# Optimization experiments

Hardware: AMD Instinct MI355X
Metric: run time of the kernel (lower is better)

## Reference

```python
import jax, jax.numpy as jnp
import numpy as np
from jax import lax

B, OBS, E, H = 65536, 20, 64, 64


def setup_inputs() -> dict:
    key = jax.random.key(0)
    ks = jax.random.split(key, 13)
    s = 0.1
    inp = {
        "obs_traj": jax.random.normal(ks[0], (B, OBS, 2), jnp.float32),
        "W_emb": jax.random.normal(ks[1], (E, 2), jnp.float32) * s,
        "b_emb": jax.random.normal(ks[2], (E,), jnp.float32) * s,
        "Wih_e": jax.random.normal(ks[3], (4 * H, E), jnp.float32) * s,
        "Whh_e": jax.random.normal(ks[4], (4 * H, H), jnp.float32) * s,
        "bih_e": jax.random.normal(ks[5], (4 * H,), jnp.float32) * s,
        "bhh_e": jax.random.normal(ks[6], (4 * H,), jnp.float32) * s,
        "Wih_d": jax.random.normal(ks[7], (4 * H, E), jnp.float32) * s,
        "Whh_d": jax.random.normal(ks[8], (4 * H, H), jnp.float32) * s,
        "bih_d": jax.random.normal(ks[9], (4 * H,), jnp.float32) * s,
        "bhh_d": jax.random.normal(ks[10], (4 * H,), jnp.float32) * s,
        "W_fc": jax.random.normal(ks[11], (2, H), jnp.float32) * s,
        "b_fc": jax.random.normal(ks[12], (2,), jnp.float32) * s,
        "pred_len": 12,
    }
    return inp


def _lstm_step(x, h, c, Wih, Whh, b):
    # PyTorch LSTM gate order: i, f, g, o
    g = x @ Wih.T + h @ Whh.T + b  # [B, 4H]
    i, f, gg, o = jnp.split(g, 4, axis=-1)
    c2 = jax.nn.sigmoid(f) * c + jax.nn.sigmoid(i) * jnp.tanh(gg)
    h2 = jax.nn.sigmoid(o) * jnp.tanh(c2)
    return h2, c2


def reference(obs_traj, W_emb, b_emb, Wih_e, Whh_e, bih_e, bhh_e,
              Wih_d, Whh_d, bih_d, bhh_d, W_fc, b_fc, pred_len):
    bsz = obs_traj.shape[0]
    dt = obs_traj.dtype
    # Encoder: embed all observed steps at once, then scan the LSTM over time.
    emb = jax.nn.relu(obs_traj @ W_emb.T + b_emb)  # [B, OBS, E]
    b_e = bih_e + bhh_e
    h0 = jnp.zeros((bsz, H), dt)
    c0 = jnp.zeros((bsz, H), dt)

    def enc_step(carry, x_t):
        h, c = carry
        h, c = _lstm_step(x_t, h, c, Wih_e, Whh_e, b_e)
        return (h, c), None

    (h, c), _ = lax.scan(enc_step, (h0, c0), jnp.swapaxes(emb, 0, 1))

    b_d = bih_d + bhh_d
    dec_in = jax.nn.relu(obs_traj[:, -1, :] @ W_emb.T + b_emb)  # [B, E]

    def dec_step(carry, _):
        h, c, x = carry
        h, c = _lstm_step(x, h, c, Wih_d, Whh_d, b_d)
        pred = h @ W_fc.T + b_fc  # [B, 2]
        nxt = jax.nn.relu(pred @ W_emb.T + b_emb)
        return (h, c, nxt), pred

    _, preds = lax.scan(dec_step, (h, c, dec_in), None, length=pred_len)
    return jnp.swapaxes(preds, 0, 1)  # [B, pred_len, 2]
```

## Files before the change

kernel.cpp:

```cpp
#include <hip/hip_runtime.h>

typedef __bf16 bf16x8 __attribute__((ext_vector_type(8)));
typedef __bf16 bf16x4 __attribute__((ext_vector_type(4)));
typedef float  f32x4  __attribute__((ext_vector_type(4)));
typedef float  f32x2  __attribute__((ext_vector_type(2)));

constexpr int BATCH = 65536;
constexpr int OBS   = 20;
constexpr int PRED  = 12;
constexpr int BT    = 64;
constexpr int AST   = 136;

constexpr float SIO = -1.4426950408889634f;
constexpr float SG  =  2.8853900817779268f;

__device__ __forceinline__ float exp2_(float x) { return __builtin_amdgcn_exp2f(x); }
__device__ __forceinline__ float rcp_(float x)  { return __builtin_amdgcn_rcpf(x); }

struct SmallW {
    float  biasf_e[256];
    float  biasf_d[256];
    float4 embc[64];
    float  wfc[128];
    float  bfc[2];
};

__global__ __launch_bounds__(256, 3)
void vanilla_lstm(const float* __restrict__ obs,
                  const float* __restrict__ W_emb, const float* __restrict__ b_emb,
                  const float* __restrict__ Wih_e, const float* __restrict__ Whh_e,
                  const float* __restrict__ bih_e, const float* __restrict__ bhh_e,
                  const float* __restrict__ Wih_d, const float* __restrict__ Whh_d,
                  const float* __restrict__ bih_d, const float* __restrict__ bhh_d,
                  const float* __restrict__ W_fc,  const float* __restrict__ b_fc,
                  float* __restrict__ out)
{
    __shared__ __align__(16) __bf16 As[BT * AST];
    __shared__ bf16x8 wkt3[1024];
    __shared__ __align__(16) float  pred_s[BT * 2];
    __shared__ SmallW sw;

    const int tid  = threadIdx.x;
    const int wv   = tid >> 6;
    const int lane = tid & 63;
    const int m    = lane & 15;
    const int q    = lane >> 4;
    const int wblk = wv * 16;
    const size_t gRow0 = (size_t)blockIdx.x * BT;

    {
        const int wv_ = tid >> 6, c_ = (tid >> 4) & 3, qr = tid & 15;
        const int g = c_ * 64 + wv_ * 16 + qr;
        const float sc = (c_ == 2) ? SG : SIO;
        sw.biasf_e[tid] = sc * (bih_e[g] + bhh_e[g]);
        sw.biasf_d[tid] = sc * (bih_d[g] + bhh_d[g]);
    }
    if (tid < 64)  sw.embc[tid] = make_float4(W_emb[2 * tid], W_emb[2 * tid + 1], b_emb[tid], 0.f);
    if (tid < 128) sw.wfc[tid]  = W_fc[tid];
    if (tid < 2)   sw.bfc[tid]  = b_fc[tid];

    {
        uint4 z; z.x = z.y = z.z = z.w = 0u;
        uint4* p = (uint4*)As;
        constexpr int NV = BT * AST * 2 / 16;
        #pragma unroll
        for (int i = 0; i < NV / 256; ++i) p[tid + i * 256] = z;
        if (tid < (NV % 256)) p[tid + (NV / 256) * 256] = z;
    }

    bf16x8 bfr[4][3];
    auto load_bfr = [&](const float* Wih, const float* Whh) {
        #pragma unroll
        for (int c = 0; c < 4; ++c) {
            const float sc = (c == 2) ? SG : SIO;
            const int n = c * 64 + wblk + m;
            #pragma unroll
            for (int kt = 0; kt < 3; ++kt) {
                const float* s = (kt < 2) ? (Wih + n * 64 + kt * 32 + q * 8)
                                          : (Whh + n * 64 + q * 8);
                float4 a = *(const float4*)s;
                float4 b = *(const float4*)(s + 4);
                bf16x8 v;
                v[0] = (__bf16)(sc * a.x); v[1] = (__bf16)(sc * a.y);
                v[2] = (__bf16)(sc * a.z); v[3] = (__bf16)(sc * a.w);
                v[4] = (__bf16)(sc * b.x); v[5] = (__bf16)(sc * b.y);
                v[6] = (__bf16)(sc * b.z); v[7] = (__bf16)(sc * b.w);
                bfr[c][kt] = v;
            }
        }
    };
    auto fill_wkt3 = [&](const float* Whh) {
        #pragma unroll
        for (int c = 0; c < 4; ++c) {
            const float sc = (c == 2) ? SG : SIO;
            const int n = c * 64 + wblk + m;
            const float* s = Whh + n * 64 + 32 + q * 8;
            float4 a = *(const float4*)s;
            float4 b = *(const float4*)(s + 4);
            bf16x8 v;
            v[0] = (__bf16)(sc * a.x); v[1] = (__bf16)(sc * a.y);
            v[2] = (__bf16)(sc * a.z); v[3] = (__bf16)(sc * a.w);
            v[4] = (__bf16)(sc * b.x); v[5] = (__bf16)(sc * b.y);
            v[6] = (__bf16)(sc * b.z); v[7] = (__bf16)(sc * b.w);
            wkt3[(wv * 4 + c) * 64 + lane] = v;
        }
    };
    load_bfr(Wih_e, Whh_e);
    fill_wkt3(Whh_e);

    f32x4 cst[4];
    #pragma unroll
    for (int i = 0; i < 4; ++i) cst[i] = f32x4{0.f, 0.f, 0.f, 0.f};

    __syncthreads();

    f32x4 acc[2][4];

    auto gemm = [&](int chunk, const float* bfrag) {
        #pragma unroll
        for (int c = 0; c < 4; ++c) {
            f32x4 b = *(const f32x4*)&bfrag[(wv * 4 + c) * 16 + q * 4];
            acc[0][c] = b;
            acc[1][c] = b;
        }
        #pragma unroll
        for (int kt = 0; kt < 3; ++kt) {
            bf16x8 af0 = *(const bf16x8*)&As[(chunk * 32 + m) * AST + kt * 32 + q * 8];
            bf16x8 af1 = *(const bf16x8*)&As[(chunk * 32 + 16 + m) * AST + kt * 32 + q * 8];
            #pragma unroll
            for (int c = 0; c < 4; ++c) {
                acc[0][c] = __builtin_amdgcn_mfma_f32_16x16x32_bf16(bfr[c][kt], af0, acc[0][c], 0, 0, 0);
                acc[1][c] = __builtin_amdgcn_mfma_f32_16x16x32_bf16(bfr[c][kt], af1, acc[1][c], 0, 0, 0);
            }
        }
        {
            bf16x8 af0 = *(const bf16x8*)&As[(chunk * 32 + m) * AST + 96 + q * 8];
            bf16x8 af1 = *(const bf16x8*)&As[(chunk * 32 + 16 + m) * AST + 96 + q * 8];
            #pragma unroll
            for (int c = 0; c < 4; ++c) {
                bf16x8 w3 = wkt3[(wv * 4 + c) * 64 + lane];
                acc[0][c] = __builtin_amdgcn_mfma_f32_16x16x32_bf16(w3, af0, acc[0][c], 0, 0, 0);
                acc[1][c] = __builtin_amdgcn_mfma_f32_16x16x32_bf16(w3, af1, acc[1][c], 0, 0, 0);
            }
        }
    };

    auto update = [&](int chunk) {
        #pragma unroll
        for (int sub = 0; sub < 2; ++sub) {
            const int idx = chunk * 2 + sub;
            const int row = chunk * 32 + sub * 16 + m;
            f32x4 ci = cst[idx];
            bf16x4 h4;
            #pragma unroll
            for (int r = 0; r < 4; ++r) {
                const float gi = acc[sub][0][r];
                const float gf = acc[sub][1][r];
                const float gg = acc[sub][2][r];
                const float go = acc[sub][3][r];
                const float Ef = exp2_(gf);
                const float a  = ci[r] * rcp_(1.0f + Ef);
                const float Ei = exp2_(gi);
                const float Eg = exp2_(gg);
                const float d1 = 1.0f + Ei;
                const float r1 = rcp_(fmaf(d1, Eg, d1));
                const float cN = fmaf(Eg - 1.0f, r1, a);
                const float Eo = exp2_(go);
                const float Ec = exp2_(cN * SG);
                const float d2 = 1.0f + Eo;
                const float r2 = rcp_(fmaf(d2, Ec, d2));
                const float h  = (Ec - 1.0f) * r2;
                ci[r] = cN;
                h4[r] = (__bf16)h;
            }
            cst[idx] = ci;
            *(bf16x4*)&As[row * AST + 64 + wblk + q * 4] = h4;
        }
    };

    auto emb_chunk = [&](int chunk, float o0, float o1) {
        const int row = chunk * 32 + (lane & 31);
        const int h8  = lane >> 5;
        bf16x8 v;
        #pragma unroll
        for (int j = 0; j < 8; ++j) {
            float4 wc = sw.embc[wblk + h8 * 8 + j];
            v[j] = (__bf16)fmaxf(fmaf(o0, wc.x, fmaf(o1, wc.y, wc.z)), 0.f);
        }
        *(bf16x8*)&As[row * AST + wblk + h8 * 8] = v;
    };

    const float* obr = obs + (gRow0 + (lane & 31)) * (OBS * 2);

    {
        f32x2 o0 = *(const f32x2*)obr;
        f32x2 o1 = *(const f32x2*)(obr + 32 * (OBS * 2));
        emb_chunk(0, o0[0], o0[1]);
        emb_chunk(1, o1[0], o1[1]);
    }
    __syncthreads();
    gemm(0, sw.biasf_e);

    for (int t = 0; t < OBS; ++t) {
        __syncthreads();
        f32x2 on0{0.f, 0.f};
        if (t + 1 < OBS) on0 = *(const f32x2*)(obr + (t + 1) * 2);
        update(0);
        gemm(1, sw.biasf_e);
        if (t + 1 < OBS) emb_chunk(0, on0[0], on0[1]);
        __syncthreads();
        f32x2 on1{0.f, 0.f};
        if (t + 1 < OBS) on1 = *(const f32x2*)(obr + 32 * (OBS * 2) + (t + 1) * 2);
        update(1);
        if (t + 1 < OBS) {
            gemm(0, sw.biasf_e);
            emb_chunk(1, on1[0], on1[1]);
        }
    }

    load_bfr(Wih_d, Whh_d);
    fill_wkt3(Whh_d);
    gemm(0, sw.biasf_d);

    auto pred_phase = [&](int chunk, int td) {
        const int row  = chunk * 32 + (tid >> 3);
        const int comp = (tid >> 2) & 1;
        const int seg  = tid & 3;
        bf16x8 h0 = *(const bf16x8*)&As[row * AST + 64 + seg * 16];
        bf16x8 h1 = *(const bf16x8*)&As[row * AST + 64 + seg * 16 + 8];
        f32x4 w0 = *(const f32x4*)&sw.wfc[comp * 64 + seg * 16];
        f32x4 w1 = *(const f32x4*)&sw.wfc[comp * 64 + seg * 16 + 4];
        f32x4 w2 = *(const f32x4*)&sw.wfc[comp * 64 + seg * 16 + 8];
        f32x4 w3 = *(const f32x4*)&sw.wfc[comp * 64 + seg * 16 + 12];
        float p = (float)h0[0] * w0[0] + (float)h0[1] * w0[1] + (float)h0[2] * w0[2] + (float)h0[3] * w0[3]
                + (float)h0[4] * w1[0] + (float)h0[5] * w1[1] + (float)h0[6] * w1[2] + (float)h0[7] * w1[3]
                + (float)h1[0] * w2[0] + (float)h1[1] * w2[1] + (float)h1[2] * w2[2] + (float)h1[3] * w2[3]
                + (float)h1[4] * w3[0] + (float)h1[5] * w3[1] + (float)h1[6] * w3[2] + (float)h1[7] * w3[3];
        p += __shfl_xor(p, 1, 64);
        p += __shfl_xor(p, 2, 64);
        if (seg == 0) {
            p += sw.bfc[comp];
            pred_s[row * 2 + comp] = p;
            out[((gRow0 + row) * PRED + td) * 2 + comp] = p;
        }
    };
    auto emb_dec = [&](int chunk) {
        const int row = chunk * 32 + (lane & 31);
        f32x2 pv = *(const f32x2*)&pred_s[row * 2];
        emb_chunk(chunk, pv[0], pv[1]);
    };

    for (int td = 0; td < PRED; ++td) {
        __syncthreads();
        update(0);
        gemm(1, sw.biasf_d);
        __syncthreads();
        update(1);
        pred_phase(0, td);
        __syncthreads();
        pred_phase(1, td);
        if (td + 1 < PRED) emb_dec(0);
        __syncthreads();
        if (td + 1 < PRED) {
            emb_dec(1);
            gemm(0, sw.biasf_d);
        }
    }
}

extern "C" void kernel_launch(void* const* d_in, const int* in_sizes, int n_in,
                              void* d_out, int out_size, void* d_ws, size_t ws_size,
                              hipStream_t stream) {
    (void)in_sizes; (void)n_in; (void)d_ws; (void)ws_size; (void)out_size;
    const float* obs   = (const float*)d_in[0];
    const float* W_emb = (const float*)d_in[1];
    const float* b_emb = (const float*)d_in[2];
    const float* Wih_e = (const float*)d_in[3];
    const float* Whh_e = (const float*)d_in[4];
    const float* bih_e = (const float*)d_in[5];
    const float* bhh_e = (const float*)d_in[6];
    const float* Wih_d = (const float*)d_in[7];
    const float* Whh_d = (const float*)d_in[8];
    const float* bih_d = (const float*)d_in[9];
    const float* bhh_d = (const float*)d_in[10];
    const float* W_fc  = (const float*)d_in[11];
    const float* b_fc  = (const float*)d_in[12];
    float* o = (float*)d_out;

    dim3 grid(BATCH / BT), block(256);
    hipLaunchKernelGGL(vanilla_lstm, grid, block, 0, stream,
                       obs, W_emb, b_emb, Wih_e, Whh_e, bih_e, bhh_e,
                       Wih_d, Whh_d, bih_d, bhh_d, W_fc, b_fc, o);
}
```

Baseline: 282.7 us.

## Split batch into mixed 96-row and 64-row blocks to balance CU load

Replaces the uniform 1024 blocks of 64 rows with 768 blocks: 512 handle 96 rows (three 16-row subtiles per chunk) and 256 handle 64 rows. The row count per block becomes a template parameter, and the GEMM, update, embedding and prediction loops are generalised over it. The aim is to cut tail waves across the 256 CUs at three blocks per CU and to amortise the per-block weight loading over more rows. The cost is more registers for the extra accumulators and state, which may threaten occupancy at the launch bound of 3, plus predicated partial-lane work in the embed and predict phases.

```diff
diff --git a/kernel.cpp b/kernel.cpp
--- a/kernel.cpp
+++ b/kernel.cpp
@@ -5,11 +5,11 @@
 typedef float  f32x4  __attribute__((ext_vector_type(4)));
 typedef float  f32x2  __attribute__((ext_vector_type(2)));
 
-constexpr int BATCH = 65536;
 constexpr int OBS   = 20;
 constexpr int PRED  = 12;
-constexpr int BT    = 64;
 constexpr int AST   = 136;
+constexpr int NBIG  = 512;
+constexpr int GRID  = 768;
 
 constexpr float SIO = -1.4426950408889634f;
 constexpr float SG  =  2.8853900817779268f;
@@ -25,76 +25,17 @@
     float  bfc[2];
 };
 
-__global__ __launch_bounds__(256, 3)
-void vanilla_lstm(const float* __restrict__ obs,
-                  const float* __restrict__ W_emb, const float* __restrict__ b_emb,
-                  const float* __restrict__ Wih_e, const float* __restrict__ Whh_e,
-                  const float* __restrict__ bih_e, const float* __restrict__ bhh_e,
-                  const float* __restrict__ Wih_d, const float* __restrict__ Whh_d,
-                  const float* __restrict__ bih_d, const float* __restrict__ bhh_d,
-                  const float* __restrict__ W_fc,  const float* __restrict__ b_fc,
-                  float* __restrict__ out)
-{
-    __shared__ __align__(16) __bf16 As[BT * AST];
-    __shared__ bf16x8 wkt3[1024];
-    __shared__ __align__(16) float  pred_s[BT * 2];
-    __shared__ SmallW sw;
-
-    const int tid  = threadIdx.x;
-    const int wv   = tid >> 6;
-    const int lane = tid & 63;
-    const int m    = lane & 15;
-    const int q    = lane >> 4;
-    const int wblk = wv * 16;
-    const size_t gRow0 = (size_t)blockIdx.x * BT;
-
-    {
-        const int wv_ = tid >> 6, c_ = (tid >> 4) & 3, qr = tid & 15;
-        const int g = c_ * 64 + wv_ * 16 + qr;
-        const float sc = (c_ == 2) ? SG : SIO;
-        sw.biasf_e[tid] = sc * (bih_e[g] + bhh_e[g]);
-        sw.biasf_d[tid] = sc * (bih_d[g] + bhh_d[g]);
-    }
-    if (tid < 64)  sw.embc[tid] = make_float4(W_emb[2 * tid], W_emb[2 * tid + 1], b_emb[tid], 0.f);
-    if (tid < 128) sw.wfc[tid]  = W_fc[tid];
-    if (tid < 2)   sw.bfc[tid]  = b_fc[tid];
-
-    {
-        uint4 z; z.x = z.y = z.z = z.w = 0u;
-        uint4* p = (uint4*)As;
-        constexpr int NV = BT * AST * 2 / 16;
-        #pragma unroll
-        for (int i = 0; i < NV / 256; ++i) p[tid + i * 256] = z;
-        if (tid < (NV % 256)) p[tid + (NV / 256) * 256] = z;
-    }
-
-    bf16x8 bfr[4][3];
-    auto load_bfr = [&](const float* Wih, const float* Whh) {
-        #pragma unroll
-        for (int c = 0; c < 4; ++c) {
-            const float sc = (c == 2) ? SG : SIO;
-            const int n = c * 64 + wblk + m;
-            #pragma unroll
-            for (int kt = 0; kt < 3; ++kt) {
-                const float* s = (kt < 2) ? (Wih + n * 64 + kt * 32 + q * 8)
-                                          : (Whh + n * 64 + q * 8);
-                float4 a = *(const float4*)s;
-                float4 b = *(const float4*)(s + 4);
-                bf16x8 v;
-                v[0] = (__bf16)(sc * a.x); v[1] = (__bf16)(sc * a.y);
-                v[2] = (__bf16)(sc * a.z); v[3] = (__bf16)(sc * a.w);
-                v[4] = (__bf16)(sc * b.x); v[5] = (__bf16)(sc * b.y);
-                v[6] = (__bf16)(sc * b.z); v[7] = (__bf16)(sc * b.w);
-                bfr[c][kt] = v;
-            }
-        }
-    };
-    auto fill_wkt3 = [&](const float* Whh) {
-        #pragma unroll
-        for (int c = 0; c < 4; ++c) {
-            const float sc = (c == 2) ? SG : SIO;
-            const int n = c * 64 + wblk + m;
-            const float* s = Whh + n * 64 + 32 + q * 8;
+__device__ __forceinline__ void load_bfr(bf16x8 (&bfr)[4][3],
+                                         const float* Wih, const float* Whh,
+                                         int wblk, int m, int q) {
+    #pragma unroll
+    for (int c = 0; c < 4; ++c) {
+        const float sc = (c == 2) ? SG : SIO;
+        const int n = c * 64 + wblk + m;
+        #pragma unroll
+        for (int kt = 0; kt < 3; ++kt) {
+            const float* s = (kt < 2) ? (Wih + n * 64 + kt * 32 + q * 8)
+                                      : (Whh + n * 64 + q * 8);
             float4 a = *(const float4*)s;
             float4 b = *(const float4*)(s + 4);
             bf16x8 v;
@@ -102,54 +43,93 @@
             v[2] = (__bf16)(sc * a.z); v[3] = (__bf16)(sc * a.w);
             v[4] = (__bf16)(sc * b.x); v[5] = (__bf16)(sc * b.y);
             v[6] = (__bf16)(sc * b.z); v[7] = (__bf16)(sc * b.w);
-            wkt3[(wv * 4 + c) * 64 + lane] = v;
-        }
-    };
-    load_bfr(Wih_e, Whh_e);
-    fill_wkt3(Whh_e);
-
-    f32x4 cst[4];
+            bfr[c][kt] = v;
+        }
+    }
+}
+
+__device__ __forceinline__ void fill_wkt3(bf16x8* wkt3, const float* Whh,
+                                          int wv, int lane, int wblk, int m, int q) {
     #pragma unroll
-    for (int i = 0; i < 4; ++i) cst[i] = f32x4{0.f, 0.f, 0.f, 0.f};
-
-    __syncthreads();
-
-    f32x4 acc[2][4];
+    for (int c = 0; c < 4; ++c) {
+        const float sc = (c == 2) ? SG : SIO;
+        const int n = c * 64 + wblk + m;
+        const float* s = Whh + n * 64 + 32 + q * 8;
+        float4 a = *(const float4*)s;
+        float4 b = *(const float4*)(s + 4);
+        bf16x8 v;
+        v[0] = (__bf16)(sc * a.x); v[1] = (__bf16)(sc * a.y);
+        v[2] = (__bf16)(sc * a.z); v[3] = (__bf16)(sc * a.w);
+        v[4] = (__bf16)(sc * b.x); v[5] = (__bf16)(sc * b.y);
+        v[6] = (__bf16)(sc * b.z); v[7] = (__bf16)(sc * b.w);
+        wkt3[(wv * 4 + c) * 64 + lane] = v;
+    }
+}
+
+template<int NSUB>
+__device__ void lstm_body(__bf16* As, bf16x8* wkt3, float* pred_s, SmallW& sw,
+                          const float* obs,
+                          const float* Wih_e, const float* Whh_e,
+                          const float* Wih_d, const float* Whh_d,
+                          float* out, size_t gRow0)
+{
+    constexpr int CH = NSUB * 16;
+    constexpr int NP = (NSUB + 1) / 2;
+    const int tid  = threadIdx.x;
+    const int wv   = tid >> 6;
+    const int lane = tid & 63;
+    const int m    = lane & 15;
+    const int q    = lane >> 4;
+    const int wblk = wv * 16;
+
+    bf16x8 bfr[4][3];
+    load_bfr(bfr, Wih_e, Whh_e, wblk, m, q);
+
+    f32x4 cst[2 * NSUB];
+    #pragma unroll
+    for (int i = 0; i < 2 * NSUB; ++i) cst[i] = f32x4{0.f, 0.f, 0.f, 0.f};
+
+    f32x4 acc[NSUB][4];
 
     auto gemm = [&](int chunk, const float* bfrag) {
         #pragma unroll
         for (int c = 0; c < 4; ++c) {
             f32x4 b = *(const f32x4*)&bfrag[(wv * 4 + c) * 16 + q * 4];
-            acc[0][c] = b;
-            acc[1][c] = b;
+            #pragma unroll
+            for (int s = 0; s < NSUB; ++s) acc[s][c] = b;
         }
         #pragma unroll
         for (int kt = 0; kt < 3; ++kt) {
-            bf16x8 af0 = *(const bf16x8*)&As[(chunk * 32 + m) * AST + kt * 32 + q * 8];
-            bf16x8 af1 = *(const bf16x8*)&As[(chunk * 32 + 16 + m) * AST + kt * 32 + q * 8];
-            #pragma unroll
-            for (int c = 0; c < 4; ++c) {
-                acc[0][c] = __builtin_amdgcn_mfma_f32_16x16x32_bf16(bfr[c][kt], af0, acc[0][c], 0, 0, 0);
-                acc[1][c] = __builtin_amdgcn_mfma_f32_16x16x32_bf16(bfr[c][kt], af1, acc[1][c], 0, 0, 0);
-            }
+            bf16x8 af[NSUB];
+            #pragma unroll
+            for (int s = 0; s < NSUB; ++s)
+                af[s] = *(const bf16x8*)&As[(chunk * CH + s * 16 + m) * AST + kt * 32 + q * 8];
+            #pragma unroll
+            for (int s = 0; s < NSUB; ++s)
+                #pragma unroll
+                for (int c = 0; c < 4; ++c)
+                    acc[s][c] = __builtin_amdgcn_mfma_f32_16x16x32_bf16(bfr[c][kt], af[s], acc[s][c], 0, 0, 0);
         }
         {
-            bf16x8 af0 = *(const bf16x8*)&As[(chunk * 32 + m) * AST + 96 + q * 8];
-            bf16x8 af1 = *(const bf16x8*)&As[(chunk * 32 + 16 + m) * AST + 96 + q * 8];
+            bf16x8 af[NSUB];
+            #pragma unroll
+            for (int s = 0; s < NSUB; ++s)
+                af[s] = *(const bf16x8*)&As[(chunk * CH + s * 16 + m) * AST + 96 + q * 8];
             #pragma unroll
             for (int c = 0; c < 4; ++c) {
                 bf16x8 w3 = wkt3[(wv * 4 + c) * 64 + lane];
-                acc[0][c] = __builtin_amdgcn_mfma_f32_16x16x32_bf16(w3, af0, acc[0][c], 0, 0, 0);
-                acc[1][c] = __builtin_amdgcn_mfma_f32_16x16x32_bf16(w3, af1, acc[1][c], 0, 0, 0);
+                #pragma unroll
+                for (int s = 0; s < NSUB; ++s)
+                    acc[s][c] = __builtin_amdgcn_mfma_f32_16x16x32_bf16(w3, af[s], acc[s][c], 0, 0, 0);
             }
         }
     };
 
     auto update = [&](int chunk) {
         #pragma unroll
-        for (int sub = 0; sub < 2; ++sub) {
-            const int idx = chunk * 2 + sub;
-            const int row = chunk * 32 + sub * 16 + m;
+        for (int sub = 0; sub < NSUB; ++sub) {
+            const int idx = chunk * NSUB + sub;
+            const int row = chunk * CH + sub * 16 + m;
             f32x4 ci = cst[idx];
             bf16x4 h4;
             #pragma unroll
@@ -178,76 +158,96 @@
         }
     };
 
-    auto emb_chunk = [&](int chunk, float o0, float o1) {
-        const int row = chunk * 32 + (lane & 31);
-        const int h8  = lane >> 5;
-        bf16x8 v;
-        #pragma unroll
-        for (int j = 0; j < 8; ++j) {
-            float4 wc = sw.embc[wblk + h8 * 8 + j];
-            v[j] = (__bf16)fmaxf(fmaf(o0, wc.x, fmaf(o1, wc.y, wc.z)), 0.f);
-        }
-        *(bf16x8*)&As[row * AST + wblk + h8 * 8] = v;
-    };
-
-    const float* obr = obs + (gRow0 + (lane & 31)) * (OBS * 2);
-
-    {
-        f32x2 o0 = *(const f32x2*)obr;
-        f32x2 o1 = *(const f32x2*)(obr + 32 * (OBS * 2));
-        emb_chunk(0, o0[0], o0[1]);
-        emb_chunk(1, o1[0], o1[1]);
-    }
+    auto emb_enc = [&](int chunk, int t) {
+        const int h8 = lane >> 5;
+        #pragma unroll
+        for (int p = 0; p < NP; ++p) {
+            const int rloc = p * 32 + (lane & 31);
+            if (rloc < CH) {
+                const int row = chunk * CH + rloc;
+                f32x2 ov = *(const f32x2*)(obs + (gRow0 + row) * (OBS * 2) + t * 2);
+                bf16x8 v;
+                #pragma unroll
+                for (int j = 0; j < 8; ++j) {
+                    float4 wc = sw.embc[wblk + h8 * 8 + j];
+                    v[j] = (__bf16)fmaxf(fmaf(ov[0], wc.x, fmaf(ov[1], wc.y, wc.z)), 0.f);
+                }
+                *(bf16x8*)&As[row * AST + wblk + h8 * 8] = v;
+            }
+        }
+    };
+
+    __syncthreads();
+
+    emb_enc(0, 0);
+    emb_enc(1, 0);
     __syncthreads();
     gemm(0, sw.biasf_e);
 
     for (int t = 0; t < OBS; ++t) {
         __syncthreads();
-        f32x2 on0{0.f, 0.f};
-        if (t + 1 < OBS) on0 = *(const f32x2*)(obr + (t + 1) * 2);
         update(0);
         gemm(1, sw.biasf_e);
-        if (t + 1 < OBS) emb_chunk(0, on0[0], on0[1]);
-        __syncthreads();
-        f32x2 on1{0.f, 0.f};
-        if (t + 1 < OBS) on1 = *(const f32x2*)(obr + 32 * (OBS * 2) + (t + 1) * 2);
+        if (t + 1 < OBS) emb_enc(0, t + 1);
+        __syncthreads();
         update(1);
         if (t + 1 < OBS) {
             gemm(0, sw.biasf_e);
-            emb_chunk(1, on1[0], on1[1]);
-        }
-    }
-
-    load_bfr(Wih_d, Whh_d);
-    fill_wkt3(Whh_d);
+            emb_enc(1, t + 1);
+        }
+    }
+
+    load_bfr(bfr, Wih_d, Whh_d, wblk, m, q);
+    fill_wkt3(wkt3, Whh_d, wv, lane, wblk, m, q);
     gemm(0, sw.biasf_d);
 
     auto pred_phase = [&](int chunk, int td) {
-        const int row  = chunk * 32 + (tid >> 3);
         const int comp = (tid >> 2) & 1;
         const int seg  = tid & 3;
-        bf16x8 h0 = *(const bf16x8*)&As[row * AST + 64 + seg * 16];
-        bf16x8 h1 = *(const bf16x8*)&As[row * AST + 64 + seg * 16 + 8];
-        f32x4 w0 = *(const f32x4*)&sw.wfc[comp * 64 + seg * 16];
-        f32x4 w1 = *(const f32x4*)&sw.wfc[comp * 64 + seg * 16 + 4];
-        f32x4 w2 = *(const f32x4*)&sw.wfc[comp * 64 + seg * 16 + 8];
-        f32x4 w3 = *(const f32x4*)&sw.wfc[comp * 64 + seg * 16 + 12];
-        float p = (float)h0[0] * w0[0] + (float)h0[1] * w0[1] + (float)h0[2] * w0[2] + (float)h0[3] * w0[3]
-                + (float)h0[4] * w1[0] + (float)h0[5] * w1[1] + (float)h0[6] * w1[2] + (float)h0[7] * w1[3]
-                + (float)h1[0] * w2[0] + (float)h1[1] * w2[1] + (float)h1[2] * w2[2] + (float)h1[3] * w2[3]
-                + (float)h1[4] * w3[0] + (float)h1[5] * w3[1] + (float)h1[6] * w3[2] + (float)h1[7] * w3[3];
-        p += __shfl_xor(p, 1, 64);
-        p += __shfl_xor(p, 2, 64);
-        if (seg == 0) {
-            p += sw.bfc[comp];
-            pred_s[row * 2 + comp] = p;
-            out[((gRow0 + row) * PRED + td) * 2 + comp] = p;
+        #pragma unroll
+        for (int p = 0; p < NP; ++p) {
+            const int rloc = p * 32 + (tid >> 3);
+            const int row  = chunk * CH + rloc;
+            const bool act = (rloc < CH);
+            float pv = 0.f;
+            if (act) {
+                bf16x8 h0 = *(const bf16x8*)&As[row * AST + 64 + seg * 16];
+                bf16x8 h1 = *(const bf16x8*)&As[row * AST + 64 + seg * 16 + 8];
+                f32x4 w0 = *(const f32x4*)&sw.wfc[comp * 64 + seg * 16];
+                f32x4 w1 = *(const f32x4*)&sw.wfc[comp * 64 + seg * 16 + 4];
+                f32x4 w2 = *(const f32x4*)&sw.wfc[comp * 64 + seg * 16 + 8];
+                f32x4 w3 = *(const f32x4*)&sw.wfc[comp * 64 + seg * 16 + 12];
+                pv = (float)h0[0] * w0[0] + (float)h0[1] * w0[1] + (float)h0[2] * w0[2] + (float)h0[3] * w0[3]
+                   + (float)h0[4] * w1[0] + (float)h0[5] * w1[1] + (float)h0[6] * w1[2] + (float)h0[7] * w1[3]
+                   + (float)h1[0] * w2[0] + (float)h1[1] * w2[1] + (float)h1[2] * w2[2] + (float)h1[3] * w2[3]
+                   + (float)h1[4] * w3[0] + (float)h1[5] * w3[1] + (float)h1[6] * w3[2] + (float)h1[7] * w3[3];
+            }
+            pv += __shfl_xor(pv, 1, 64);
+            pv += __shfl_xor(pv, 2, 64);
+            if (act && seg == 0) {
+                pv += sw.bfc[comp];
+                pred_s[row * 2 + comp] = pv;
+                out[((gRow0 + row) * PRED + td) * 2 + comp] = pv;
+            }
         }
     };
     auto emb_dec = [&](int chunk) {
-        const int row = chunk * 32 + (lane & 31);
-        f32x2 pv = *(const f32x2*)&pred_s[row * 2];
-        emb_chunk(chunk, pv[0], pv[1]);
+        const int h8 = lane >> 5;
+        #pragma unroll
+        for (int p = 0; p < NP; ++p) {
+            const int rloc = p * 32 + (lane & 31);
+            if (rloc < CH) {
+                const int row = chunk * CH + rloc;
+                f32x2 pv = *(const f32x2*)&pred_s[row * 2];
+                bf16x8 v;
+                #pragma unroll
+                for (int j = 0; j < 8; ++j) {
+                    float4 wc = sw.embc[wblk + h8 * 8 + j];
+                    v[j] = (__bf16)fmaxf(fmaf(pv[0], wc.x, fmaf(pv[1], wc.y, wc.z)), 0.f);
+                }
+                *(bf16x8*)&As[row * AST + wblk + h8 * 8] = v;
+            }
+        }
     };
 
     for (int td = 0; td < PRED; ++td) {
@@ -265,6 +265,59 @@
             emb_dec(1);
             gemm(0, sw.biasf_d);
         }
+    }
+}
+
+__global__ __launch_bounds__(256, 3)
+void vanilla_lstm(const float* __restrict__ obs,
+                  const float* __restrict__ W_emb, const float* __restrict__ b_emb,
+                  const float* __restrict__ Wih_e, const float* __restrict__ Whh_e,
+                  const float* __restrict__ bih_e, const float* __restrict__ bhh_e,
+                  const float* __restrict__ Wih_d, const float* __restrict__ Whh_d,
+                  const float* __restrict__ bih_d, const float* __restrict__ bhh_d,
+                  const float* __restrict__ W_fc,  const float* __restrict__ b_fc,
+                  float* __restrict__ out)
+{
+    __shared__ __align__(16) __bf16 As[96 * AST];
+    __shared__ bf16x8 wkt3[1024];
+    __shared__ __align__(16) float  pred_s[96 * 2];
+    __shared__ SmallW sw;
+
+    const int tid = threadIdx.x;
+
+    {
+        const int wv_ = tid >> 6, c_ = (tid >> 4) & 3, qr = tid & 15;
+        const int g = c_ * 64 + wv_ * 16 + qr;
+        const float sc = (c_ == 2) ? SG : SIO;
+        sw.biasf_e[tid] = sc * (bih_e[g] + bhh_e[g]);
+        sw.biasf_d[tid] = sc * (bih_d[g] + bhh_d[g]);
+    }
+    if (tid < 64)  sw.embc[tid] = make_float4(W_emb[2 * tid], W_emb[2 * tid + 1], b_emb[tid], 0.f);
+    if (tid < 128) sw.wfc[tid]  = W_fc[tid];
+    if (tid < 2)   sw.bfc[tid]  = b_fc[tid];
+
+    {
+        uint4 z; z.x = z.y = z.z = z.w = 0u;
+        #pragma unroll
+        for (int i = 0; i < 3; ++i) {
+            const int idx = tid + i * 256;
+            const int r = idx >> 3, o = idx & 7;
+            *((uint4*)&As[r * AST + 64] + o) = z;
+        }
+    }
+
+    {
+        const int wv = tid >> 6, lane = tid & 63, m = lane & 15, q = lane >> 4;
+        fill_wkt3(wkt3, Whh_e, wv, lane, wv * 16, m, q);
+    }
+
+    const int bid = blockIdx.x;
+    if (bid < NBIG) {
+        lstm_body<3>(As, wkt3, pred_s, sw, obs, Wih_e, Whh_e, Wih_d, Whh_d,
+                     out, (size_t)bid * 96);
+    } else {
+        lstm_body<2>(As, wkt3, pred_s, sw, obs, Wih_e, Whh_e, Wih_d, Whh_d,
+                     out, (size_t)NBIG * 96 + (size_t)(bid - NBIG) * 64);
     }
 }
 
@@ -287,7 +340,7 @@
     const float* b_fc  = (const float*)d_in[12];
     float* o = (float*)d_out;
 
-    dim3 grid(BATCH / BT), block(256);
+    dim3 grid(GRID), block(256);
     hipLaunchKernelGGL(vanilla_lstm, grid, block, 0, stream,
                        obs, W_emb, b_emb, Wih_e, Whh_e, bih_e, bhh_e,
                        Wih_d, Whh_d, bih_d, bhh_d, W_fc, b_fc, o);
```

Measured after the change: 278.4 us. About the same (-1.5%).

## Double-buffer LSTM x/h tiles in LDS to cut encoder barriers to one per step

Applied to the files above, without the earlier changes.

Widens the LDS activation row so that x and h each get two ping-pong slots. In the encoder, each step now runs gemm and update for both chunks back to back, embeds the next observation into the other slot, and uses a single barrier per step instead of two. The cost is twice the LDS for activations, which may lower occupancy. The encoder also loses the old overlap of next-chunk gemm with the current chunk's update.

```diff
diff --git a/kernel.cpp b/kernel.cpp
--- a/kernel.cpp
+++ b/kernel.cpp
@@ -5,11 +5,10 @@
 typedef float  f32x4  __attribute__((ext_vector_type(4)));
 typedef float  f32x2  __attribute__((ext_vector_type(2)));
 
-constexpr int BATCH = 65536;
-constexpr int OBS   = 20;
-constexpr int PRED  = 12;
-constexpr int BT    = 64;
-constexpr int AST   = 136;
+constexpr int OBS  = 20;
+constexpr int PRED = 12;
+constexpr int BT   = 64;
+constexpr int AST  = 264;
 
 constexpr float SIO = -1.4426950408889634f;
 constexpr float SG  =  2.8853900817779268f;
@@ -24,6 +23,47 @@
     float  wfc[128];
     float  bfc[2];
 };
+
+__device__ __forceinline__ void load_bfr(bf16x8 (&bfr)[4][3],
+                                         const float* Wih, const float* Whh,
+                                         int wblk, int m, int q) {
+    #pragma unroll
+    for (int c = 0; c < 4; ++c) {
+        const float sc = (c == 2) ? SG : SIO;
+        const int n = c * 64 + wblk + m;
+        #pragma unroll
+        for (int kt = 0; kt < 3; ++kt) {
+            const float* s = (kt < 2) ? (Wih + n * 64 + kt * 32 + q * 8)
+                                      : (Whh + n * 64 + q * 8);
+            float4 a = *(const float4*)s;
+            float4 b = *(const float4*)(s + 4);
+            bf16x8 v;
+            v[0] = (__bf16)(sc * a.x); v[1] = (__bf16)(sc * a.y);
+            v[2] = (__bf16)(sc * a.z); v[3] = (__bf16)(sc * a.w);
+            v[4] = (__bf16)(sc * b.x); v[5] = (__bf16)(sc * b.y);
+            v[6] = (__bf16)(sc * b.z); v[7] = (__bf16)(sc * b.w);
+            bfr[c][kt] = v;
+        }
+    }
+}
+
+__device__ __forceinline__ void fill_wkt3(bf16x8* wkt3, const float* Whh,
+                                          int wv, int lane, int wblk, int m, int q) {
+    #pragma unroll
+    for (int c = 0; c < 4; ++c) {
+        const float sc = (c == 2) ? SG : SIO;
+        const int n = c * 64 + wblk + m;
+        const float* s = Whh + n * 64 + 32 + q * 8;
+        float4 a = *(const float4*)s;
+        float4 b = *(const float4*)(s + 4);
+        bf16x8 v;
+        v[0] = (__bf16)(sc * a.x); v[1] = (__bf16)(sc * a.y);
+        v[2] = (__bf16)(sc * a.z); v[3] = (__bf16)(sc * a.w);
+        v[4] = (__bf16)(sc * b.x); v[5] = (__bf16)(sc * b.y);
+        v[6] = (__bf16)(sc * b.z); v[7] = (__bf16)(sc * b.w);
+        wkt3[(wv * 4 + c) * 64 + lane] = v;
+    }
+}
 
 __global__ __launch_bounds__(256, 3)
 void vanilla_lstm(const float* __restrict__ obs,
@@ -37,7 +77,7 @@
 {
     __shared__ __align__(16) __bf16 As[BT * AST];
     __shared__ bf16x8 wkt3[1024];
-    __shared__ __align__(16) float  pred_s[BT * 2];
+    __shared__ __align__(16) float pred_s[BT * 2];
     __shared__ SmallW sw;
 
     const int tid  = threadIdx.x;
@@ -61,72 +101,36 @@
 
     {
         uint4 z; z.x = z.y = z.z = z.w = 0u;
-        uint4* p = (uint4*)As;
-        constexpr int NV = BT * AST * 2 / 16;
-        #pragma unroll
-        for (int i = 0; i < NV / 256; ++i) p[tid + i * 256] = z;
-        if (tid < (NV % 256)) p[tid + (NV / 256) * 256] = z;
+        #pragma unroll
+        for (int i = 0; i < 4; ++i) {
+            const int idx = tid + i * 256;
+            const int r = idx >> 4, o = idx & 15;
+            *((uint4*)&As[r * AST + 128] + o) = z;
+        }
     }
 
     bf16x8 bfr[4][3];
-    auto load_bfr = [&](const float* Wih, const float* Whh) {
-        #pragma unroll
-        for (int c = 0; c < 4; ++c) {
-            const float sc = (c == 2) ? SG : SIO;
-            const int n = c * 64 + wblk + m;
-            #pragma unroll
-            for (int kt = 0; kt < 3; ++kt) {
-                const float* s = (kt < 2) ? (Wih + n * 64 + kt * 32 + q * 8)
-                                          : (Whh + n * 64 + q * 8);
-                float4 a = *(const float4*)s;
-                float4 b = *(const float4*)(s + 4);
-                bf16x8 v;
-                v[0] = (__bf16)(sc * a.x); v[1] = (__bf16)(sc * a.y);
-                v[2] = (__bf16)(sc * a.z); v[3] = (__bf16)(sc * a.w);
-                v[4] = (__bf16)(sc * b.x); v[5] = (__bf16)(sc * b.y);
-                v[6] = (__bf16)(sc * b.z); v[7] = (__bf16)(sc * b.w);
-                bfr[c][kt] = v;
-            }
-        }
-    };
-    auto fill_wkt3 = [&](const float* Whh) {
-        #pragma unroll
-        for (int c = 0; c < 4; ++c) {
-            const float sc = (c == 2) ? SG : SIO;
-            const int n = c * 64 + wblk + m;
-            const float* s = Whh + n * 64 + 32 + q * 8;
-            float4 a = *(const float4*)s;
-            float4 b = *(const float4*)(s + 4);
-            bf16x8 v;
-            v[0] = (__bf16)(sc * a.x); v[1] = (__bf16)(sc * a.y);
-            v[2] = (__bf16)(sc * a.z); v[3] = (__bf16)(sc * a.w);
-            v[4] = (__bf16)(sc * b.x); v[5] = (__bf16)(sc * b.y);
-            v[6] = (__bf16)(sc * b.z); v[7] = (__bf16)(sc * b.w);
-            wkt3[(wv * 4 + c) * 64 + lane] = v;
-        }
-    };
-    load_bfr(Wih_e, Whh_e);
-    fill_wkt3(Whh_e);
+    load_bfr(bfr, Wih_e, Whh_e, wblk, m, q);
+    fill_wkt3(wkt3, Whh_e, wv, lane, wblk, m, q);
 
     f32x4 cst[4];
     #pragma unroll
     for (int i = 0; i < 4; ++i) cst[i] = f32x4{0.f, 0.f, 0.f, 0.f};
 
-    __syncthreads();
-
     f32x4 acc[2][4];
 
-    auto gemm = [&](int chunk, const float* bfrag) {
+    auto gemm = [&](int chunk, int xb, int hb, const float* bfrag) {
         #pragma unroll
         for (int c = 0; c < 4; ++c) {
             f32x4 b = *(const f32x4*)&bfrag[(wv * 4 + c) * 16 + q * 4];
             acc[0][c] = b;
             acc[1][c] = b;
         }
+        const int base[3] = { xb, xb + 32, hb };
         #pragma unroll
         for (int kt = 0; kt < 3; ++kt) {
-            bf16x8 af0 = *(const bf16x8*)&As[(chunk * 32 + m) * AST + kt * 32 + q * 8];
-            bf16x8 af1 = *(const bf16x8*)&As[(chunk * 32 + 16 + m) * AST + kt * 32 + q * 8];
+            bf16x8 af0 = *(const bf16x8*)&As[(chunk * 32 + m) * AST + base[kt] + q * 8];
+            bf16x8 af1 = *(const bf16x8*)&As[(chunk * 32 + 16 + m) * AST + base[kt] + q * 8];
             #pragma unroll
             for (int c = 0; c < 4; ++c) {
                 acc[0][c] = __builtin_amdgcn_mfma_f32_16x16x32_bf16(bfr[c][kt], af0, acc[0][c], 0, 0, 0);
@@ -134,8 +138,8 @@
             }
         }
         {
-            bf16x8 af0 = *(const bf16x8*)&As[(chunk * 32 + m) * AST + 96 + q * 8];
-            bf16x8 af1 = *(const bf16x8*)&As[(chunk * 32 + 16 + m) * AST + 96 + q * 8];
+            bf16x8 af0 = *(const bf16x8*)&As[(chunk * 32 + m) * AST + hb + 32 + q * 8];
+            bf16x8 af1 = *(const bf16x8*)&As[(chunk * 32 + 16 + m) * AST + hb + 32 + q * 8];
             #pragma unroll
             for (int c = 0; c < 4; ++c) {
                 bf16x8 w3 = wkt3[(wv * 4 + c) * 64 + lane];
@@ -145,7 +149,7 @@
         }
     };
 
-    auto update = [&](int chunk) {
+    auto update = [&](int chunk, int hw) {
         #pragma unroll
         for (int sub = 0; sub < 2; ++sub) {
             const int idx = chunk * 2 + sub;
@@ -174,60 +178,56 @@
                 h4[r] = (__bf16)h;
             }
             cst[idx] = ci;
-            *(bf16x4*)&As[row * AST + 64 + wblk + q * 4] = h4;
-        }
-    };
-
-    auto emb_chunk = [&](int chunk, float o0, float o1) {
+            *(bf16x4*)&As[row * AST + hw + wblk + q * 4] = h4;
+        }
+    };
+
+    auto emb_enc = [&](int chunk, int t, int xw) {
         const int row = chunk * 32 + (lane & 31);
         const int h8  = lane >> 5;
+        f32x2 ov = *(const f32x2*)(obs + (gRow0 + row) * (OBS * 2) + t * 2);
         bf16x8 v;
         #pragma unroll
         for (int j = 0; j < 8; ++j) {
             float4 wc = sw.embc[wblk + h8 * 8 + j];
-            v[j] = (__bf16)fmaxf(fmaf(o0, wc.x, fmaf(o1, wc.y, wc.z)), 0.f);
-        }
-        *(bf16x8*)&As[row * AST + wblk + h8 * 8] = v;
-    };
-
-    const float* obr = obs + (gRow0 + (lane & 31)) * (OBS * 2);
-
-    {
-        f32x2 o0 = *(const f32x2*)obr;
-        f32x2 o1 = *(const f32x2*)(obr + 32 * (OBS * 2));
-        emb_chunk(0, o0[0], o0[1]);
-        emb_chunk(1, o1[0], o1[1]);
-    }
+            v[j] = (__bf16)fmaxf(fmaf(ov[0], wc.x, fmaf(ov[1], wc.y, wc.z)), 0.f);
+        }
+        *(bf16x8*)&As[row * AST + xw + wblk + h8 * 8] = v;
+    };
+
     __syncthreads();
-    gemm(0, sw.biasf_e);
+
+    emb_enc(0, 0, 0);
+    emb_enc(1, 0, 0);
+    __syncthreads();
 
     for (int t = 0; t < OBS; ++t) {
-        __syncthreads();
-        f32x2 on0{0.f, 0.f};
-        if (t + 1 < OBS) on0 = *(const f32x2*)(obr + (t + 1) * 2);
-        update(0);
-        gemm(1, sw.biasf_e);
-        if (t + 1 < OBS) emb_chunk(0, on0[0], on0[1]);
-        __syncthreads();
-        f32x2 on1{0.f, 0.f};
-        if (t + 1 < OBS) on1 = *(const f32x2*)(obr + 32 * (OBS * 2) + (t + 1) * 2);
-        update(1);
+        const int xb = (t & 1) * 64;
+        const int hb = 128 + (t & 1) * 64;
+        const int hw = 128 + ((t + 1) & 1) * 64;
+        gemm(0, xb, hb, sw.biasf_e);
+        update(0, hw);
+        gemm(1, xb, hb, sw.biasf_e);
+        update(1, hw);
         if (t + 1 < OBS) {
-            gemm(0, sw.biasf_e);
-            emb_chunk(1, on1[0], on1[1]);
-        }
-    }
-
-    load_bfr(Wih_d, Whh_d);
-    fill_wkt3(Whh_d);
-    gemm(0, sw.biasf_d);
+            const int xw = ((t + 1) & 1) * 64;
+            emb_enc(0, t + 1, xw);
+            emb_enc(1, t + 1, xw);
+        }
+        __syncthreads();
+    }
+
+    load_bfr(bfr, Wih_d, Whh_d, wblk, m, q);
+    fill_wkt3(wkt3, Whh_d, wv, lane, wblk, m, q);
+    gemm(0, 64, 128, sw.biasf_d);
 
     auto pred_phase = [&](int chunk, int td) {
+        const int hro  = 128 + ((td + 1) & 1) * 64;
         const int row  = chunk * 32 + (tid >> 3);
         const int comp = (tid >> 2) & 1;
         const int seg  = tid & 3;
-        bf16x8 h0 = *(const bf16x8*)&As[row * AST + 64 + seg * 16];
-        bf16x8 h1 = *(const bf16x8*)&As[row * AST + 64 + seg * 16 + 8];
+        bf16x8 h0 = *(const bf16x8*)&As[row * AST + hro + seg * 16];
+        bf16x8 h1 = *(const bf16x8*)&As[row * AST + hro + seg * 16 + 8];
         f32x4 w0 = *(const f32x4*)&sw.wfc[comp * 64 + seg * 16];
         f32x4 w1 = *(const f32x4*)&sw.wfc[comp * 64 + seg * 16 + 4];
         f32x4 w2 = *(const f32x4*)&sw.wfc[comp * 64 + seg * 16 + 8];
@@ -244,26 +244,37 @@
             out[((gRow0 + row) * PRED + td) * 2 + comp] = p;
         }
     };
-    auto emb_dec = [&](int chunk) {
+    auto emb_dec = [&](int chunk, int xw) {
         const int row = chunk * 32 + (lane & 31);
+        const int h8  = lane >> 5;
         f32x2 pv = *(const f32x2*)&pred_s[row * 2];
-        emb_chunk(chunk, pv[0], pv[1]);
+        bf16x8 v;
+        #pragma unroll
+        for (int j = 0; j < 8; ++j) {
+            float4 wc = sw.embc[wblk + h8 * 8 + j];
+            v[j] = (__bf16)fmaxf(fmaf(pv[0], wc.x, fmaf(pv[1], wc.y, wc.z)), 0.f);
+        }
+        *(bf16x8*)&As[row * AST + xw + wblk + h8 * 8] = v;
     };
 
     for (int td = 0; td < PRED; ++td) {
-        __syncthreads();
-        update(0);
-        gemm(1, sw.biasf_d);
-        __syncthreads();
-        update(1);
+        const int xb = ((td + 1) & 1) * 64;
+        const int hb = 128 + (td & 1) * 64;
+        const int hw = 128 + ((td + 1) & 1) * 64;
+        const int xw = (td & 1) * 64;
+        __syncthreads();
+        update(0, hw);
+        gemm(1, xb, hb, sw.biasf_d);
+        __syncthreads();
+        update(1, hw);
         pred_phase(0, td);
         __syncthreads();
         pred_phase(1, td);
-        if (td + 1 < PRED) emb_dec(0);
+        if (td + 1 < PRED) emb_dec(0, xw);
         __syncthreads();
         if (td + 1 < PRED) {
-            emb_dec(1);
-            gemm(0, sw.biasf_d);
+            emb_dec(1, xw);
+            gemm(0, ((td + 2) & 1) * 64, 128 + ((td + 1) & 1) * 64, sw.biasf_d);
         }
     }
 }
@@ -287,7 +298,7 @@
     const float* b_fc  = (const float*)d_in[12];
     float* o = (float*)d_out;
 
-    dim3 grid(BATCH / BT), block(256);
+    dim3 grid(65536 / BT), block(256);
     hipLaunchKernelGGL(vanilla_lstm, grid, block, 0, stream,
                        obs, W_emb, b_emb, Wih_e, Whh_e, bih_e, bhh_e,
                        Wih_d, Whh_d, bih_d, bhh_d, W_fc, b_fc, o);
```

Measured after the change: 298.7 us. 5.7% more time.
